# Optimization experiments

Hardware: AMD Instinct MI355X
Metric: run time of the kernel (lower is better)

## Reference

```python
import jax, jax.numpy as jnp
import numpy as np

B, Y, X, C = 32, 32, 32, 256
N, K = 8, 4            # query heads, kv groups
M = N // K             # query heads per group
DQ, DV = 32, 32        # qk / v head widths (invariant rep)
HQ = DQ // 2           # rotation pairs


def setup_inputs() -> dict:
    key = jax.random.key(0)
    ks = jax.random.split(key, 8)
    s = 1.0 / np.sqrt(C)
    return {
        'x':    jax.random.normal(ks[0], (B, Y, X, C), jnp.float32),
        'xpos': jax.random.uniform(ks[1], (X, 2), jnp.float32),
        'ypos': jax.random.uniform(ks[2], (Y, 2), jnp.float32),
        'Wq':   jax.random.normal(ks[3], (C, 2, 2, 2, M, K, HQ, 2), jnp.float32) * s,
        'Wk':   jax.random.normal(ks[4], (C, 2, 2, 2, K, HQ, 2), jnp.float32) * s,
        'Wv':   jax.random.normal(ks[5], (C, 2, 2, 2, K, DV), jnp.float32) * s,
        'bv':   jnp.zeros((2, 2, 2, K, DV), jnp.float32),
        'Wo':   jax.random.normal(ks[6], (2, 2, 2, M, K, DV, C), jnp.float32) / np.sqrt(8 * N * DV),
        'rope_freq': jax.random.normal(ks[7], (M, K, HQ, 2), jnp.float32),
    }


def _rope_scaling():
    # pi / stack([linspace(1,30,HQ), linspace(0.1,1,HQ)]).T -> [HQ, 2]
    return jnp.asarray(np.pi / np.stack([np.linspace(1.0, 30.0, HQ),
                                         np.linspace(0.1, 1.0, HQ)], axis=-1).astype(np.float32))


def _rot(freq, pos):
    # freq [M,K,HQ,2], pos [L,2] -> rotation matrices [L, 2(dir), M, K, HQ, 2, 2]
    phi = jnp.einsum('mkhp,lp->lmkh', freq, pos)
    c, s = jnp.cos(phi), jnp.sin(phi)
    # idx = [[[0,2],[1,0]],[[0,1],[2,0]]] over (cos, sin, -sin): fwd and inverse rotation
    r_fwd = jnp.stack([jnp.stack([c, -s], -1), jnp.stack([s, c], -1)], -2)
    r_bwd = jnp.stack([jnp.stack([c, s], -1), jnp.stack([-s, c], -1)], -2)
    return jnp.stack([r_fwd, r_bwd], axis=1)


def reference(x, xpos, ypos, Wq, Wk, Wv, bv, Wo, rope_freq):
    freq = rope_freq * _rope_scaling()                       # [M,K,HQ,2]
    # projections: a=axis(2), d=direction(2), v=chirality(2)
    q = jnp.einsum('byxc,cadvmkhp->byxadvmkhp', x, Wq)
    k = jnp.einsum('byxc,cadvkhp->byxadvkhp', x, Wk)
    vv = jnp.einsum('byxc,cadvkh->byxadvkh', x, Wv) + bv

    outs = []
    for axis, pos in ((0, ypos), (1, xpos)):
        rot = _rot(freq, pos)                                # [L,d,M,K,HQ,2,2]
        qa = q[:, :, :, axis]                                # [B,Y,X,d,v,M,K,HQ,2]
        ka = k[:, :, :, axis]                                # [B,Y,X,d,v,K,HQ,2]
        va = vv[:, :, :, axis]                               # [B,Y,X,d,v,K,DV]
        if axis == 0:  # attend along Y
            Qr = jnp.einsum('byxdvmkhp,ydmkhpq->byxdvmkhq', qa, rot)
            Kr = jnp.einsum('byxdvkhp,ydmkhpq->byxdvmkhq', ka, rot)
            sc = jax.nn.sigmoid(jnp.einsum('btxdvmkhq,bsxdvmkhq->btsxdvmk', Qr, Kr))
            o = jnp.einsum('btsxdvmk,bsxdvkh->btxdvmkh', sc, va)
        else:          # attend along X
            Qr = jnp.einsum('byxdvmkhp,xdmkhpq->byxdvmkhq', qa, rot)
            Kr = jnp.einsum('byxdvkhp,xdmkhpq->byxdvmkhq', ka, rot)
            sc = jax.nn.sigmoid(jnp.einsum('bytdvmkhq,bysdvmkhq->bytsdvmk', Qr, Kr))
            o = jnp.einsum('bytsdvmk,bysdvkh->bytdvmkh', sc, va)
        outs.append(o)                                       # [B,Y,X,d,v,M,K,DV]
    V = jnp.stack(outs, axis=3)                              # [B,Y,X,a,d,v,M,K,DV]
    return jnp.einsum('byxadvmkh,advmkhc->byxc', V, Wo)
```

## Files before the change

kernel.cpp:

```cpp
#include <hip/hip_runtime.h>
#include <math.h>

namespace {

typedef __attribute__((ext_vector_type(8))) short short8;
typedef __attribute__((ext_vector_type(4))) float f32x4;

constexpr float kPI = 3.14159265358979323846f;

__device__ __forceinline__ unsigned short f2bf(float f) {
    unsigned int u = __float_as_uint(f);
    u += 0x7fffu + ((u >> 16) & 1u);
    return (unsigned short)(u >> 16);
}

__device__ __forceinline__ short8 pack8(const float* f) {
    short8 r;
    #pragma unroll
    for (int i = 0; i < 8; ++i) r[i] = (short)f2bf(f[i]);
    return r;
}

__device__ __forceinline__ f32x4 MFMA(short8 a, short8 b, f32x4 c) {
    return __builtin_amdgcn_mfma_f32_16x16x32_bf16(a, b, c, 0, 0, 0);
}

__global__ __launch_bounds__(256)
void prep_weights(const float* __restrict__ Wq, const float* __restrict__ Wk,
                  const float* __restrict__ Wv, const float* __restrict__ Wo,
                  short* __restrict__ wsQ, short* __restrict__ wsKV,
                  short* __restrict__ wsO)
{
    const int cid = blockIdx.x * 4 + (threadIdx.x >> 6);
    const int l = threadIdx.x & 63;
    const int lr = l & 15, lk = l >> 4;
    const int arr = cid >> 10, c2 = cid & 1023;
    const int adv = c2 >> 7, ks = (c2 >> 4) & 7, nt = c2 & 15;
    const int c0 = ks * 32 + lk * 8;
    float v[8];
    if (arr == 0) {
        const int j = nt * 16 + lr;
        #pragma unroll
        for (int i = 0; i < 8; ++i)
            v[i] = Wq[((size_t)(c0 + i) * 8 + adv) * 256 + j];
    } else if (arr == 1) {
        if (nt < 8) {
            const int j = nt * 16 + lr;
            #pragma unroll
            for (int i = 0; i < 8; ++i)
                v[i] = Wk[((size_t)(c0 + i) * 8 + adv) * 128 + j];
        } else {
            const int j = (nt - 8) * 16 + lr;
            #pragma unroll
            for (int i = 0; i < 8; ++i)
                v[i] = Wv[((size_t)(c0 + i) * 8 + adv) * 128 + j];
        }
    } else {
        const int cc = nt * 16 + lr;
        #pragma unroll
        for (int i = 0; i < 8; ++i)
            v[i] = Wo[((size_t)adv * 256 + (c0 + i)) * 256 + cc];
    }
    short* dst = (arr == 0 ? wsQ : arr == 1 ? wsKV : wsO) + (size_t)c2 * 512 + l * 8;
    *(short8*)dst = pack8(v);
}

template <int AXIS, bool ACCUM>
__global__ __launch_bounds__(512, 4)
void axial_attn_mfma(const float* __restrict__ x,
                     const float* __restrict__ xpos,
                     const float* __restrict__ ypos,
                     const float* __restrict__ bvp,
                     const float* __restrict__ rfreq,
                     const short* __restrict__ wsQ,
                     const short* __restrict__ wsKV,
                     const short* __restrict__ wsO,
                     float* __restrict__ out)
{
    __shared__ __align__(16) short xs[32 * 256];
    __shared__ __align__(16) short qbuf[32 * 256];
    __shared__ __align__(16) short kbuf[32 * 256];
    __shared__ __align__(16) short vbuf[4 * 32 * 32];
    __shared__ __align__(16) short obuf[32 * 256];
    __shared__ float2 posf[32];
    __shared__ float2 rfs[128];

    const int t = threadIdx.x;
    const int b = blockIdx.x >> 5;
    const int line = blockIdx.x & 31;
    const int w = t >> 6, l = t & 63;
    const int lr = l & 15, lk = l >> 4;
    const int p01 = l & 1;

    {
        const int row = t >> 4;
        const int c0 = (t & 15) * 16;
        const int gy = (AXIS == 0) ? row : line;
        const int gx = (AXIS == 0) ? line : row;
        const float* px = x + ((size_t)((b * 32 + gy) * 32 + gx)) * 256 + c0;
        float tmp[16];
        #pragma unroll
        for (int i = 0; i < 16; i += 4) {
            const float4 a = *(const float4*)(px + i);
            tmp[i] = a.x; tmp[i + 1] = a.y; tmp[i + 2] = a.z; tmp[i + 3] = a.w;
        }
        const int swz = (row & 7) << 3;
        *(short8*)&xs[row * 256 + (c0 ^ swz)] = pack8(tmp);
        *(short8*)&xs[row * 256 + ((c0 + 8) ^ swz)] = pack8(tmp + 8);
    }
    const float* posv = (AXIS == 0) ? ypos : xpos;
    if (t < 128) {
        const int h = t & 15;
        const float s0 = kPI / (1.0f + (29.0f / 15.0f) * (float)h);
        const float s1 = kPI / (0.1f + 0.06f * (float)h);
        rfs[t] = make_float2(rfreq[2 * t] * s0, rfreq[2 * t + 1] * s1);
    }
    if (t < 32) posf[t] = make_float2(posv[2 * t], posv[2 * t + 1]);
    __syncthreads();

    f32x4 oacc[2][2] = {};
    const short8* wsQv  = (const short8*)wsQ;
    const short8* wsKVv = (const short8*)wsKV;
    const short8* wsOv  = (const short8*)wsO;
    const int m_w = w >> 2, kk_w = w & 3;
    const int aswz = (lr & 7) << 3;

    for (int dvi = 0; dvi < 4; ++dvi) {
        const int adv = AXIS * 4 + dvi;
        const float sgn = (dvi < 2) ? 1.0f : -1.0f;

        {
            f32x4 acc[2][2] = {};
            #pragma unroll 2
            for (int ks = 0; ks < 8; ++ks) {
                const int e = (ks * 32 + lk * 8) ^ aswz;
                const short8 a0 = *(const short8*)&xs[lr * 256 + e];
                const short8 a1 = *(const short8*)&xs[(16 + lr) * 256 + e];
                const short8 b0 = wsQv[(size_t)((adv * 8 + ks) * 16 + w * 2 + 0) * 64 + l];
                const short8 b1 = wsQv[(size_t)((adv * 8 + ks) * 16 + w * 2 + 1) * 64 + l];
                acc[0][0] = MFMA(a0, b0, acc[0][0]);
                acc[1][0] = MFMA(a1, b0, acc[1][0]);
                acc[0][1] = MFMA(a0, b1, acc[0][1]);
                acc[1][1] = MFMA(a1, b1, acc[1][1]);
            }
            #pragma unroll
            for (int mt = 0; mt < 2; ++mt)
                #pragma unroll
                for (int nt = 0; nt < 2; ++nt) {
                    const int h = (nt * 16 + lr) >> 1;
                    const float2 rf = rfs[m_w * 64 + kk_w * 16 + h];
                    #pragma unroll
                    for (int r = 0; r < 4; ++r) {
                        const float own = acc[mt][nt][r];
                        const float oth = __shfl_xor(own, 1);
                        const int pos = mt * 16 + lk * 4 + r;
                        const float2 pp = posf[pos];
                        float sv, cv;
                        __sincosf(rf.x * pp.x + rf.y * pp.y, &sv, &cv);
                        const float rv = (p01 == 0) ? cv * own + sgn * sv * oth
                                                    : cv * own - sgn * sv * oth;
                        const int col = w * 32 + nt * 16 + lr;
                        qbuf[pos * 256 + (col ^ ((pos & 7) << 3))] = (short)f2bf(rv);
                    }
                }
        }

        {
            f32x4 acc[2][2] = {};
            #pragma unroll 2
            for (int ks = 0; ks < 8; ++ks) {
                const int e = (ks * 32 + lk * 8) ^ aswz;
                const short8 a0 = *(const short8*)&xs[lr * 256 + e];
                const short8 a1 = *(const short8*)&xs[(16 + lr) * 256 + e];
                const short8 b0 = wsKVv[(size_t)((adv * 8 + ks) * 16 + w * 2 + 0) * 64 + l];
                const short8 b1 = wsKVv[(size_t)((adv * 8 + ks) * 16 + w * 2 + 1) * 64 + l];
                acc[0][0] = MFMA(a0, b0, acc[0][0]);
                acc[1][0] = MFMA(a1, b0, acc[1][0]);
                acc[0][1] = MFMA(a0, b1, acc[0][1]);
                acc[1][1] = MFMA(a1, b1, acc[1][1]);
            }
            if (w < 4) {
                #pragma unroll
                for (int mt = 0; mt < 2; ++mt)
                    #pragma unroll
                    for (int nt = 0; nt < 2; ++nt) {
                        const int h = (nt * 16 + lr) >> 1;
                        const float2 rf0 = rfs[w * 16 + h];
                        const float2 rf1 = rfs[64 + w * 16 + h];
                        #pragma unroll
                        for (int r = 0; r < 4; ++r) {
                            const float own = acc[mt][nt][r];
                            const float oth = __shfl_xor(own, 1);
                            const int pos = mt * 16 + lk * 4 + r;
                            const float2 pp = posf[pos];
                            #pragma unroll
                            for (int m2 = 0; m2 < 2; ++m2) {
                                const float2 rf = (m2 == 0) ? rf0 : rf1;
                                float sv, cv;
                                __sincosf(rf.x * pp.x + rf.y * pp.y, &sv, &cv);
                                const float rv = (p01 == 0) ? cv * own + sgn * sv * oth
                                                            : cv * own - sgn * sv * oth;
                                const int col = (m2 * 4 + w) * 32 + nt * 16 + lr;
                                kbuf[pos * 256 + (col ^ ((pos & 7) << 3))] = (short)f2bf(rv);
                            }
                        }
                    }
            } else {
                const int kk = w - 4;
                #pragma unroll
                for (int nt = 0; nt < 2; ++nt) {
                    const int dv = nt * 16 + lr;
                    const float bvv = bvp[adv * 128 + kk * 32 + dv];
                    #pragma unroll
                    for (int mt = 0; mt < 2; ++mt)
                        #pragma unroll
                        for (int r = 0; r < 4; ++r) {
                            const int s = mt * 16 + lk * 4 + r;
                            vbuf[kk * 1024 + dv * 32 + (s ^ ((dv & 3) << 3))] =
                                (short)f2bf(acc[mt][nt][r] + bvv);
                        }
                }
            }
        }
        __syncthreads();

        {
            const int g = w;
            short8 ka[2], qa[2];
            #pragma unroll
            for (int st = 0; st < 2; ++st) {
                const int row = st * 16 + lr;
                ka[st] = *(const short8*)&kbuf[row * 256 + ((g * 32 + lk * 8) ^ ((row & 7) << 3))];
            }
            #pragma unroll
            for (int qt = 0; qt < 2; ++qt) {
                const int row = qt * 16 + lr;
                qa[qt] = *(const short8*)&qbuf[row * 256 + ((g * 32 + lk * 8) ^ ((row & 7) << 3))];
            }
            f32x4 d[2][2] = {};
            #pragma unroll
            for (int st = 0; st < 2; ++st)
                #pragma unroll
                for (int qt = 0; qt < 2; ++qt)
                    d[st][qt] = MFMA(ka[st], qa[qt], d[st][qt]);

            unsigned int pk[2][2][2];
            #pragma unroll
            for (int st = 0; st < 2; ++st)
                #pragma unroll
                for (int qt = 0; qt < 2; ++qt)
                    #pragma unroll
                    for (int h2 = 0; h2 < 2; ++h2) {
                        const float za = __builtin_amdgcn_rcpf(1.0f + __expf(-d[st][qt][2 * h2]));
                        const float zb = __builtin_amdgcn_rcpf(1.0f + __expf(-d[st][qt][2 * h2 + 1]));
                        pk[st][qt][h2] = (unsigned int)f2bf(za) |
                                         ((unsigned int)f2bf(zb) << 16);
                    }

            const int srcA = ((lk & 1) * 2) * 16 + lr;
            short8 pa[2];
            #pragma unroll
            for (int qt = 0; qt < 2; ++qt) {
                union { unsigned int u[4]; short8 s; } uu;
                #pragma unroll
                for (int jp = 0; jp < 4; ++jp) {
                    const int src = srcA + (jp >> 1) * 16;
                    const int v0 = __shfl((int)pk[0][qt][jp & 1], src, 64);
                    const int v1 = __shfl((int)pk[1][qt][jp & 1], src, 64);
                    uu.u[jp] = (lk < 2) ? (unsigned int)v0 : (unsigned int)v1;
                }
                pa[qt] = uu.s;
            }

            const int kkg = g & 3;
            short8 vb2[2];
            #pragma unroll
            for (int dvt = 0; dvt < 2; ++dvt) {
                const int dv = dvt * 16 + lr;
                vb2[dvt] = *(const short8*)&vbuf[kkg * 1024 + dv * 32 + ((lk * 8) ^ ((dv & 3) << 3))];
            }
            f32x4 o2[2][2] = {};
            #pragma unroll
            for (int qt = 0; qt < 2; ++qt)
                #pragma unroll
                for (int dvt = 0; dvt < 2; ++dvt)
                    o2[qt][dvt] = MFMA(pa[qt], vb2[dvt], o2[qt][dvt]);

            #pragma unroll
            for (int qt = 0; qt < 2; ++qt)
                #pragma unroll
                for (int dvt = 0; dvt < 2; ++dvt)
                    #pragma unroll
                    for (int r = 0; r < 4; ++r) {
                        const int q = qt * 16 + lk * 4 + r;
                        const int col = g * 32 + dvt * 16 + lr;
                        obuf[q * 256 + (col ^ ((q & 7) << 3))] = (short)f2bf(o2[qt][dvt][r]);
                    }
        }
        __syncthreads();

        {
            #pragma unroll 2
            for (int ks = 0; ks < 8; ++ks) {
                const int e = (ks * 32 + lk * 8) ^ aswz;
                const short8 a0 = *(const short8*)&obuf[lr * 256 + e];
                const short8 a1 = *(const short8*)&obuf[(16 + lr) * 256 + e];
                const short8 b0 = wsOv[(size_t)((adv * 8 + ks) * 16 + w * 2 + 0) * 64 + l];
                const short8 b1 = wsOv[(size_t)((adv * 8 + ks) * 16 + w * 2 + 1) * 64 + l];
                oacc[0][0] = MFMA(a0, b0, oacc[0][0]);
                oacc[1][0] = MFMA(a1, b0, oacc[1][0]);
                oacc[0][1] = MFMA(a0, b1, oacc[0][1]);
                oacc[1][1] = MFMA(a1, b1, oacc[1][1]);
            }
        }
    }

    #pragma unroll
    for (int mt = 0; mt < 2; ++mt)
        #pragma unroll
        for (int nt = 0; nt < 2; ++nt)
            #pragma unroll
            for (int r = 0; r < 4; ++r) {
                const int pos = mt * 16 + lk * 4 + r;
                const int c = w * 32 + nt * 16 + lr;
                const int gy = (AXIS == 0) ? pos : line;
                const int gx = (AXIS == 0) ? line : pos;
                float* po = out + ((size_t)((b * 32 + gy) * 32 + gx)) * 256 + c;
                if (ACCUM) *po += oacc[mt][nt][r];
                else       *po = oacc[mt][nt][r];
            }
}

}

extern "C" void kernel_launch(void* const* d_in, const int* in_sizes, int n_in,
                              void* d_out, int out_size, void* d_ws, size_t ws_size,
                              hipStream_t stream) {
    (void)in_sizes; (void)n_in; (void)out_size; (void)ws_size;
    const float* x     = (const float*)d_in[0];
    const float* xpos  = (const float*)d_in[1];
    const float* ypos  = (const float*)d_in[2];
    const float* Wq    = (const float*)d_in[3];
    const float* Wk    = (const float*)d_in[4];
    const float* Wv    = (const float*)d_in[5];
    const float* bv    = (const float*)d_in[6];
    const float* Wo    = (const float*)d_in[7];
    const float* rfreq = (const float*)d_in[8];
    float* out = (float*)d_out;

    short* wsQ  = (short*)d_ws;
    short* wsKV = wsQ + 1024 * 512;
    short* wsO  = wsKV + 1024 * 512;

    prep_weights<<<dim3(768), dim3(256), 0, stream>>>(Wq, Wk, Wv, Wo, wsQ, wsKV, wsO);
    axial_attn_mfma<0, false><<<dim3(1024), dim3(512), 0, stream>>>(
        x, xpos, ypos, bv, rfreq, wsQ, wsKV, wsO, out);
    axial_attn_mfma<1, true><<<dim3(1024), dim3(512), 0, stream>>>(
        x, xpos, ypos, bv, rfreq, wsQ, wsKV, wsO, out);
}
```

Measured before the change: 287.0 us.

## Precompute RoPE cos/sin table in LDS as half2 and reuse qbuf for output

Builds a per-block table of cos/sin values, one per position and frequency, stored as half2 in shared memory once at kernel start. This replaces the repeated __sincosf calls in the Q and K rotation loops, which were recomputed for every dvi iteration, with table lookups. The obuf buffer is dropped and its role is taken by qbuf, with an extra barrier per iteration so the next iteration cannot overwrite qbuf while it is still being read. Together these cut transcendental work and LDS footprint, at the cost of fp16 precision on cos/sin and one added sync per loop.

```diff
diff --git a/kernel.cpp b/kernel.cpp
--- a/kernel.cpp
+++ b/kernel.cpp
@@ -1,4 +1,5 @@
 #include <hip/hip_runtime.h>
+#include <hip/hip_fp16.h>
 #include <math.h>
 
 namespace {
@@ -81,9 +82,7 @@
     __shared__ __align__(16) short qbuf[32 * 256];
     __shared__ __align__(16) short kbuf[32 * 256];
     __shared__ __align__(16) short vbuf[4 * 32 * 32];
-    __shared__ __align__(16) short obuf[32 * 256];
-    __shared__ float2 posf[32];
-    __shared__ float2 rfs[128];
+    __shared__ __half2 csl2[32 * 128];
 
     const int t = threadIdx.x;
     const int b = blockIdx.x >> 5;
@@ -109,13 +108,17 @@
         *(short8*)&xs[row * 256 + ((c0 + 8) ^ swz)] = pack8(tmp + 8);
     }
     const float* posv = (AXIS == 0) ? ypos : xpos;
-    if (t < 128) {
-        const int h = t & 15;
+    for (int idx = t; idx < 32 * 128; idx += 512) {
+        const int pos = idx >> 7, r = idx & 127;
+        const int h = r & 15;
         const float s0 = kPI / (1.0f + (29.0f / 15.0f) * (float)h);
         const float s1 = kPI / (0.1f + 0.06f * (float)h);
-        rfs[t] = make_float2(rfreq[2 * t] * s0, rfreq[2 * t + 1] * s1);
+        const float phi = rfreq[r * 2 + 0] * s0 * posv[pos * 2 + 0] +
+                          rfreq[r * 2 + 1] * s1 * posv[pos * 2 + 1];
+        float sv, cv;
+        __sincosf(phi, &sv, &cv);
+        csl2[pos * 128 + (r ^ (pos & 15))] = __floats2half2_rn(cv, sv);
     }
-    if (t < 32) posf[t] = make_float2(posv[2 * t], posv[2 * t + 1]);
     __syncthreads();
 
     f32x4 oacc[2][2] = {};
@@ -148,15 +151,13 @@
                 #pragma unroll
                 for (int nt = 0; nt < 2; ++nt) {
                     const int h = (nt * 16 + lr) >> 1;
-                    const float2 rf = rfs[m_w * 64 + kk_w * 16 + h];
                     #pragma unroll
                     for (int r = 0; r < 4; ++r) {
                         const float own = acc[mt][nt][r];
                         const float oth = __shfl_xor(own, 1);
                         const int pos = mt * 16 + lk * 4 + r;
-                        const float2 pp = posf[pos];
-                        float sv, cv;
-                        __sincosf(rf.x * pp.x + rf.y * pp.y, &sv, &cv);
+                        const __half2 csh = csl2[pos * 128 + ((m_w * 64 + kk_w * 16 + h) ^ (pos & 15))];
+                        const float cv = __low2float(csh), sv = __high2float(csh);
                         const float rv = (p01 == 0) ? cv * own + sgn * sv * oth
                                                     : cv * own - sgn * sv * oth;
                         const int col = w * 32 + nt * 16 + lr;
@@ -185,19 +186,15 @@
                     #pragma unroll
                     for (int nt = 0; nt < 2; ++nt) {
                         const int h = (nt * 16 + lr) >> 1;
-                        const float2 rf0 = rfs[w * 16 + h];
-                        const float2 rf1 = rfs[64 + w * 16 + h];
                         #pragma unroll
                         for (int r = 0; r < 4; ++r) {
                             const float own = acc[mt][nt][r];
                             const float oth = __shfl_xor(own, 1);
                             const int pos = mt * 16 + lk * 4 + r;
-                            const float2 pp = posf[pos];
                             #pragma unroll
                             for (int m2 = 0; m2 < 2; ++m2) {
-                                const float2 rf = (m2 == 0) ? rf0 : rf1;
-                                float sv, cv;
-                                __sincosf(rf.x * pp.x + rf.y * pp.y, &sv, &cv);
+                                const __half2 csh = csl2[pos * 128 + ((m2 * 64 + w * 16 + h) ^ (pos & 15))];
+                                const float cv = __low2float(csh), sv = __high2float(csh);
                                 const float rv = (p01 == 0) ? cv * own + sgn * sv * oth
                                                             : cv * own - sgn * sv * oth;
                                 const int col = (m2 * 4 + w) * 32 + nt * 16 + lr;
@@ -294,7 +291,7 @@
                     for (int r = 0; r < 4; ++r) {
                         const int q = qt * 16 + lk * 4 + r;
                         const int col = g * 32 + dvt * 16 + lr;
-                        obuf[q * 256 + (col ^ ((q & 7) << 3))] = (short)f2bf(o2[qt][dvt][r]);
+                        qbuf[q * 256 + (col ^ ((q & 7) << 3))] = (short)f2bf(o2[qt][dvt][r]);
                     }
         }
         __syncthreads();
@@ -303,8 +300,8 @@
             #pragma unroll 2
             for (int ks = 0; ks < 8; ++ks) {
                 const int e = (ks * 32 + lk * 8) ^ aswz;
-                const short8 a0 = *(const short8*)&obuf[lr * 256 + e];
-                const short8 a1 = *(const short8*)&obuf[(16 + lr) * 256 + e];
+                const short8 a0 = *(const short8*)&qbuf[lr * 256 + e];
+                const short8 a1 = *(const short8*)&qbuf[(16 + lr) * 256 + e];
                 const short8 b0 = wsOv[(size_t)((adv * 8 + ks) * 16 + w * 2 + 0) * 64 + l];
                 const short8 b1 = wsOv[(size_t)((adv * 8 + ks) * 16 + w * 2 + 1) * 64 + l];
                 oacc[0][0] = MFMA(a0, b0, oacc[0][0]);
@@ -313,6 +310,7 @@
                 oacc[1][1] = MFMA(a1, b1, oacc[1][1]);
             }
         }
+        __syncthreads();
     }
 
     #pragma unroll
```

Measured after the change: 403.4 us. +40.5%, slower.
